# Kernel tuning notes

Measured on AMD Instinct MI355X. Metric: run time of the kernel, lower is better.

The kernel has to match this reference:

```python
import jax, jax.numpy as jnp
import numpy as np

B, C, H, W = 8, 128, 256, 256
WS = 8          # window_size (square)
HEADS = 4


def setup_inputs() -> dict:
    key = jax.random.key(0)
    k1, k2, k3, k4 = jax.random.split(key, 4)
    x = jax.random.normal(k1, (B, C, H, W), dtype=jnp.float32)
    # 1x1 convs are per-pixel matmuls; store weights as [out, in]
    w_qkv = jax.random.normal(k2, (3 * C, C), dtype=jnp.float32) * 0.05   # qkv conv, bias=False
    w_proj = jax.random.normal(k3, (C, C), dtype=jnp.float32) * 0.05      # proj conv weight
    b_proj = jax.random.normal(k4, (C,), dtype=jnp.float32) * 0.01        # proj conv bias
    return {"x": x, "w_qkv": w_qkv, "w_proj": w_proj, "b_proj": b_proj}


def reference(x, w_qkv, w_proj, b_proj):
    b, c, h, w = x.shape
    ws, heads = WS, HEADS
    d = c // heads
    scale = d ** -0.5
    hn, wn = h // ws, w // ws
    n = ws * ws  # tokens per window

    # unfold with kernel=stride=ws -> row-major window partition
    # [B,C,H,W] -> [B*hn*wn, C, n]
    xw = x.reshape(b, c, hn, ws, wn, ws)
    xw = xw.transpose(0, 2, 4, 1, 3, 5).reshape(b * hn * wn, c, n)

    # 1x1 conv QKV projection (no bias)
    qkv = jnp.einsum('oc,bcn->bon', w_qkv, xw)  # [Bw, 3C, n]
    q, k, v = jnp.split(qkv, 3, axis=1)
    q = q.reshape(-1, heads, d, n)
    k = k.reshape(-1, heads, d, n)
    v = v.reshape(-1, heads, d, n)

    # attn = (q^T k) * scale, softmax over keys
    attn = jax.nn.softmax(jnp.einsum('bhdn,bhdm->bhnm', q, k) * scale, axis=-1)
    out = jnp.einsum('bhnm,bhdm->bhdn', attn, v).reshape(-1, c, n)  # [Bw, C, n]

    # 1x1 proj conv with bias
    out = jnp.einsum('oc,bcn->bon', w_proj, out) + b_proj[None, :, None]

    # fold windows back: [Bw, C, n] -> [B, C, H, W]
    out = out.reshape(b, hn, wn, c, ws, ws)
    out = out.transpose(0, 3, 1, 4, 2, 5).reshape(b, c, h, w)
    return out
```

## Files before the change

### kernel.cpp

```cpp
#include <hip/hip_runtime.h>


#define HH    256
#define WWID  256
#define SCALE 0.17677669529663687f

typedef float  f32x4  __attribute__((ext_vector_type(4)));
typedef __bf16 bf16x8 __attribute__((ext_vector_type(8)));
typedef short  s16x4  __attribute__((ext_vector_type(4)));
typedef unsigned short ushort_t;

#define SCR_BASE 16384

__device__ __forceinline__ ushort_t f2bf(float x) {
  unsigned u = __float_as_uint(x);
  u += 0x7fffu + ((u >> 16) & 1u);
  return (ushort_t)(u >> 16);
}

__global__ void prep_weights(const float* __restrict__ wqkv,
                             const float* __restrict__ wproj,
                             ushort_t* __restrict__ wbf) {
  int i = blockIdx.x * 256 + threadIdx.x;
  float v = (i < 49152) ? wqkv[i] : wproj[i - 49152];
  wbf[i] = f2bf(v);
}

__global__ __launch_bounds__(256, 2)
void winattn_main(const float* __restrict__ x,
                  const ushort_t* __restrict__ wqkv,
                  const ushort_t* __restrict__ wproj,
                  const float* __restrict__ bproj,
                  float* __restrict__ out) {
  __shared__ __align__(16) char smem[32768];

  const int tid  = threadIdx.x;
  const int lane = tid & 63;
  const int wv   = tid >> 6;
  const int l15  = lane & 15;
  const int l4   = lane >> 4;

  const int bid = blockIdx.x;
  const int win = ((bid & 7) << 10) | (bid >> 3);
  const int b   = win >> 10;
  const int wy  = (win >> 5) & 31;
  const int wx  = win & 31;
  const int gy0 = wy * 8, gx0 = wx * 8;

  #pragma unroll
  for (int it = 0; it < 4; ++it) {
    int idx   = tid + it * 256;
    int cpair = idx >> 4;
    int r     = idx & 15;
    int ty    = r >> 1, tx4 = r & 1;
    const float* px = x + (((size_t)(b * 128 + 2 * cpair) * HH + gy0 + ty) * WWID + gx0 + tx4 * 4);
    float4 v0 = *(const float4*)px;
    float4 v1 = *(const float4*)(px + (size_t)HH * WWID);
    float a0[4] = {v0.x, v0.y, v0.z, v0.w};
    float a1[4] = {v1.x, v1.y, v1.z, v1.w};
    #pragma unroll
    for (int i = 0; i < 4; ++i) {
      int tok = ty * 8 + tx4 * 4 + i;
      unsigned wword = (unsigned)f2bf(a0[i]) | ((unsigned)f2bf(a1[i]) << 16);
      int byte = (tok * 256 + cpair * 4) ^ ((tok & 7) << 4);
      *(unsigned*)(smem + byte) = wword;
    }
  }
  __syncthreads();

  const int scr = SCR_BASE + wv * 4096;
  bf16x8 bk[4], aq[4], bv[2][2];

  #define XT_AFRAG(mt, kt) \
    (*(const bf16x8*)(smem + ((((mt) * 16 + l15) * 256 + ((kt) * 32 + l4 * 8) * 2) ^ \
                              ((((mt) * 16 + l15) & 7) << 4))))

  #pragma unroll
  for (int nt2 = 0; nt2 < 2; ++nt2) {
    int orow0 = 128 + wv * 32 + nt2 * 16;
    f32x4 acc[4] = {};
    #pragma unroll
    for (int kt = 0; kt < 4; ++kt) {
      bf16x8 bf = *(const bf16x8*)(wqkv + (size_t)(orow0 + l15) * 128 + kt * 32 + l4 * 8);
      #pragma unroll
      for (int mt = 0; mt < 4; ++mt)
        acc[mt] = __builtin_amdgcn_mfma_f32_16x16x32_bf16(XT_AFRAG(mt, kt), bf, acc[mt], 0, 0, 0);
    }
    int dloc = nt2 * 16 + l15;
    #pragma unroll
    for (int mt = 0; mt < 4; ++mt)
      #pragma unroll
      for (int r = 0; r < 4; ++r) {
        int tok  = mt * 16 + l4 * 4 + r;
        int byte = scr + ((tok * 64 + dloc * 2) ^ ((tok & 3) << 4));
        *(ushort_t*)(smem + byte) = f2bf(acc[mt][r]);
      }
  }
  #pragma unroll
  for (int mtS = 0; mtS < 4; ++mtS) {
    int m    = mtS * 16 + l15;
    int byte = scr + ((m * 64 + l4 * 16) ^ ((m & 3) << 4));
    bk[mtS] = *(const bf16x8*)(smem + byte);
  }
  #pragma unroll
  for (int nt2 = 0; nt2 < 2; ++nt2) {
    int orow0 = wv * 32 + nt2 * 16;
    f32x4 acc[4] = {};
    #pragma unroll
    for (int kt = 0; kt < 4; ++kt) {
      bf16x8 bf = *(const bf16x8*)(wqkv + (size_t)(orow0 + l15) * 128 + kt * 32 + l4 * 8);
      #pragma unroll
      for (int mt = 0; mt < 4; ++mt)
        acc[mt] = __builtin_amdgcn_mfma_f32_16x16x32_bf16(XT_AFRAG(mt, kt), bf, acc[mt], 0, 0, 0);
    }
    int dloc = nt2 * 16 + l15;
    #pragma unroll
    for (int mt = 0; mt < 4; ++mt)
      #pragma unroll
      for (int r = 0; r < 4; ++r) {
        int tok  = mt * 16 + l4 * 4 + r;
        int byte = scr + ((tok * 64 + dloc * 2) ^ ((tok & 3) << 4));
        *(ushort_t*)(smem + byte) = f2bf(acc[mt][r] * SCALE);
      }
  }
  #pragma unroll
  for (int t = 0; t < 4; ++t) {
    int tok  = t * 16 + l15;
    int byte = scr + ((tok * 64 + l4 * 16) ^ ((tok & 3) << 4));
    aq[t] = *(const bf16x8*)(smem + byte);
  }
  #pragma unroll
  for (int nt2 = 0; nt2 < 2; ++nt2) {
    int orow0 = 256 + wv * 32 + nt2 * 16;
    f32x4 acc[4] = {};
    #pragma unroll
    for (int kt = 0; kt < 4; ++kt) {
      bf16x8 bf = *(const bf16x8*)(wqkv + (size_t)(orow0 + l15) * 128 + kt * 32 + l4 * 8);
      #pragma unroll
      for (int mt = 0; mt < 4; ++mt)
        acc[mt] = __builtin_amdgcn_mfma_f32_16x16x32_bf16(XT_AFRAG(mt, kt), bf, acc[mt], 0, 0, 0);
    }
    int dloc = nt2 * 16 + l15;
    #pragma unroll
    for (int mt = 0; mt < 4; ++mt) {
      int tok0 = mt * 16 + l4 * 4;
      s16x4 wv4;
      #pragma unroll
      for (int r = 0; r < 4; ++r) wv4[r] = (short)f2bf(acc[mt][r]);
      int byte = scr + ((dloc * 128 + tok0 * 2) ^ ((dloc & 7) << 4));
      *(s16x4*)(smem + byte) = wv4;
    }
  }
  #pragma unroll
  for (int vt = 0; vt < 2; ++vt)
    #pragma unroll
    for (int kt = 0; kt < 2; ++kt) {
      int d    = vt * 16 + l15;
      int byte = scr + ((d * 128 + (kt * 32 + l4 * 8) * 2) ^ ((d & 7) << 4));
      bv[vt][kt] = *(const bf16x8*)(smem + byte);
    }

  f32x4 oacc[2][2][2] = {};
  #pragma unroll
  for (int hf = 0; hf < 2; ++hf) {
    #pragma unroll
    for (int qt = 0; qt < 2; ++qt) {
      f32x4 s[4];
      #pragma unroll
      for (int mtS = 0; mtS < 4; ++mtS) {
        f32x4 z = {0.f, 0.f, 0.f, 0.f};
        s[mtS] = __builtin_amdgcn_mfma_f32_16x16x32_bf16(aq[hf * 2 + qt], bk[mtS], z, 0, 0, 0);
      }
      #pragma unroll
      for (int r = 0; r < 4; ++r) {
        float v0 = s[0][r], v1 = s[1][r], v2 = s[2][r], v3 = s[3][r];
        float mx = fmaxf(fmaxf(v0, v1), fmaxf(v2, v3));
        mx = fmaxf(mx, __shfl_xor(mx, 1));
        mx = fmaxf(mx, __shfl_xor(mx, 2));
        mx = fmaxf(mx, __shfl_xor(mx, 4));
        mx = fmaxf(mx, __shfl_xor(mx, 8));
        float e0 = __expf(v0 - mx), e1 = __expf(v1 - mx);
        float e2 = __expf(v2 - mx), e3 = __expf(v3 - mx);
        float sm = e0 + e1 + e2 + e3;
        sm += __shfl_xor(sm, 1);
        sm += __shfl_xor(sm, 2);
        sm += __shfl_xor(sm, 4);
        sm += __shfl_xor(sm, 8);
        float inv = 1.0f / sm;
        int nl = qt * 16 + l4 * 4 + r;
        int sw = (nl & 7) << 4;
        *(ushort_t*)(smem + scr + ((nl * 128 + (0 * 16 + l15) * 2) ^ sw)) = f2bf(e0 * inv);
        *(ushort_t*)(smem + scr + ((nl * 128 + (1 * 16 + l15) * 2) ^ sw)) = f2bf(e1 * inv);
        *(ushort_t*)(smem + scr + ((nl * 128 + (2 * 16 + l15) * 2) ^ sw)) = f2bf(e2 * inv);
        *(ushort_t*)(smem + scr + ((nl * 128 + (3 * 16 + l15) * 2) ^ sw)) = f2bf(e3 * inv);
      }
    }
    #pragma unroll
    for (int kt = 0; kt < 2; ++kt)
      #pragma unroll
      for (int rt = 0; rt < 2; ++rt) {
        int nl   = rt * 16 + l15;
        int byte = scr + ((nl * 128 + (kt * 32 + l4 * 8) * 2) ^ ((nl & 7) << 4));
        bf16x8 ap = *(const bf16x8*)(smem + byte);
        #pragma unroll
        for (int vt = 0; vt < 2; ++vt)
          oacc[hf][rt][vt] =
              __builtin_amdgcn_mfma_f32_16x16x32_bf16(ap, bv[vt][kt], oacc[hf][rt][vt], 0, 0, 0);
      }
  }
  __syncthreads();

  #pragma unroll
  for (int hf = 0; hf < 2; ++hf)
    #pragma unroll
    for (int rt = 0; rt < 2; ++rt)
      #pragma unroll
      for (int vt = 0; vt < 2; ++vt)
        #pragma unroll
        for (int r = 0; r < 4; ++r) {
          int tok  = hf * 32 + rt * 16 + l4 * 4 + r;
          int c    = wv * 32 + vt * 16 + l15;
          int byte = (tok * 256 + c * 2) ^ ((tok & 7) << 4);
          *(ushort_t*)(smem + byte) = f2bf(oacc[hf][rt][vt][r]);
        }
  __syncthreads();

  f32x4 pacc[2][4];
  #pragma unroll
  for (int i = 0; i < 2; ++i) {
    #pragma unroll
    for (int mt = 0; mt < 4; ++mt) pacc[i][mt] = (f32x4){0.f, 0.f, 0.f, 0.f};
    int orow0 = (wv * 2 + i) * 16;
    #pragma unroll
    for (int kt = 0; kt < 4; ++kt) {
      bf16x8 bf = *(const bf16x8*)(wproj + (size_t)(orow0 + l15) * 128 + kt * 32 + l4 * 8);
      #pragma unroll
      for (int mt = 0; mt < 4; ++mt)
        pacc[i][mt] = __builtin_amdgcn_mfma_f32_16x16x32_bf16(XT_AFRAG(mt, kt), bf, pacc[i][mt], 0, 0, 0);
    }
  }

  #pragma unroll
  for (int half = 0; half < 2; ++half) {
    __syncthreads();
    #pragma unroll
    for (int i = 0; i < 2; ++i) {
      int o = (wv * 2 + i) * 16 + l15;
      #pragma unroll
      for (int m2 = 0; m2 < 2; ++m2)
        #pragma unroll
        for (int r = 0; r < 4; ++r) {
          int ytok = m2 * 16 + l4 * 4 + r;
          int byte = SCR_BASE + ((ytok * 512 + o * 4) ^ ((ytok & 7) << 4));
          *(float*)(smem + byte) = pacc[i][half * 2 + m2][r];
        }
    }
    __syncthreads();
    #pragma unroll
    for (int it = 0; it < 2; ++it) {
      int idx = tid + it * 256;
      int o   = idx & 127;
      int ty  = idx >> 7;
      float bias = bproj[o];
      float vals[8];
      #pragma unroll
      for (int tx = 0; tx < 8; ++tx) {
        int ytok = ty * 8 + tx;
        int byte = SCR_BASE + ((ytok * 512 + o * 4) ^ ((ytok & 7) << 4));
        vals[tx] = *(const float*)(smem + byte) + bias;
      }
      int row = half * 4 + ty;
      float4 f0 = {vals[0], vals[1], vals[2], vals[3]};
      float4 f1 = {vals[4], vals[5], vals[6], vals[7]};
      float* po = out + (((size_t)(b * 128 + o) * HH + gy0 + row) * WWID + gx0);
      *(float4*)po       = f0;
      *(float4*)(po + 4) = f1;
    }
  }
}

extern "C" void kernel_launch(void* const* d_in, const int* in_sizes, int n_in,
                              void* d_out, int out_size, void* d_ws, size_t ws_size,
                              hipStream_t stream) {
  const float* x     = (const float*)d_in[0];
  const float* wqkv  = (const float*)d_in[1];
  const float* wproj = (const float*)d_in[2];
  const float* bproj = (const float*)d_in[3];
  float* out = (float*)d_out;

  ushort_t* wbf = (ushort_t*)d_ws;
  prep_weights<<<256, 256, 0, stream>>>(wqkv, wproj, wbf);
  winattn_main<<<8192, 256, 0, stream>>>(x, wbf, wbf + 49152, bproj, out);
}
```

Baseline: 297.6 us.

## Fuse Q/K projection, transpose MFMA operands, and write output directly from accumulators

Computes Q and K projections in one pass that shares the x fragments, and swaps the MFMA operand order so accumulator lanes hold contiguous token runs. That enables vectorized bf16x4 LDS stores and a softmax that reduces in registers with only two cross-lane shuffles. The attention scale is folded into the Q weights during weight prep, and native __bf16 conversions replace manual rounding. The projection epilogue now writes float4 values straight to global memory, removing the LDS staging round trip and its barriers. The cost is higher register pressure from holding accQ and accK together, plus less coalesced output stores.

```diff
diff --git a/kernel.cpp b/kernel.cpp
--- a/kernel.cpp
+++ b/kernel.cpp
@@ -7,29 +7,24 @@
 
 typedef float  f32x4  __attribute__((ext_vector_type(4)));
 typedef __bf16 bf16x8 __attribute__((ext_vector_type(8)));
-typedef short  s16x4  __attribute__((ext_vector_type(4)));
-typedef unsigned short ushort_t;
+typedef __bf16 bf16x4 __attribute__((ext_vector_type(4)));
+typedef __bf16 bf16x2 __attribute__((ext_vector_type(2)));
 
 #define SCR_BASE 16384
-
-__device__ __forceinline__ ushort_t f2bf(float x) {
-  unsigned u = __float_as_uint(x);
-  u += 0x7fffu + ((u >> 16) & 1u);
-  return (ushort_t)(u >> 16);
-}
 
 __global__ void prep_weights(const float* __restrict__ wqkv,
                              const float* __restrict__ wproj,
-                             ushort_t* __restrict__ wbf) {
+                             __bf16* __restrict__ wbf) {
   int i = blockIdx.x * 256 + threadIdx.x;
   float v = (i < 49152) ? wqkv[i] : wproj[i - 49152];
-  wbf[i] = f2bf(v);
+  if (i < 16384) v *= SCALE;
+  wbf[i] = (__bf16)v;
 }
 
 __global__ __launch_bounds__(256, 2)
 void winattn_main(const float* __restrict__ x,
-                  const ushort_t* __restrict__ wqkv,
-                  const ushort_t* __restrict__ wproj,
+                  const __bf16* __restrict__ wqkv,
+                  const __bf16* __restrict__ wproj,
                   const float* __restrict__ bproj,
                   float* __restrict__ out) {
   __shared__ __align__(16) char smem[32768];
@@ -61,9 +56,9 @@
     #pragma unroll
     for (int i = 0; i < 4; ++i) {
       int tok = ty * 8 + tx4 * 4 + i;
-      unsigned wword = (unsigned)f2bf(a0[i]) | ((unsigned)f2bf(a1[i]) << 16);
+      bf16x2 w2 = {(__bf16)a0[i], (__bf16)a1[i]};
       int byte = (tok * 256 + cpair * 4) ^ ((tok & 7) << 4);
-      *(unsigned*)(smem + byte) = wword;
+      *(bf16x2*)(smem + byte) = w2;
     }
   }
   __syncthreads();
@@ -75,124 +70,133 @@
     (*(const bf16x8*)(smem + ((((mt) * 16 + l15) * 256 + ((kt) * 32 + l4 * 8) * 2) ^ \
                               ((((mt) * 16 + l15) & 7) << 4))))
 
-  #pragma unroll
-  for (int nt2 = 0; nt2 < 2; ++nt2) {
-    int orow0 = 128 + wv * 32 + nt2 * 16;
-    f32x4 acc[4] = {};
+  {
+    f32x4 accQ[2][4] = {}, accK[2][4] = {};
     #pragma unroll
     for (int kt = 0; kt < 4; ++kt) {
-      bf16x8 bf = *(const bf16x8*)(wqkv + (size_t)(orow0 + l15) * 128 + kt * 32 + l4 * 8);
-      #pragma unroll
-      for (int mt = 0; mt < 4; ++mt)
-        acc[mt] = __builtin_amdgcn_mfma_f32_16x16x32_bf16(XT_AFRAG(mt, kt), bf, acc[mt], 0, 0, 0);
-    }
-    int dloc = nt2 * 16 + l15;
-    #pragma unroll
-    for (int mt = 0; mt < 4; ++mt)
-      #pragma unroll
-      for (int r = 0; r < 4; ++r) {
-        int tok  = mt * 16 + l4 * 4 + r;
-        int byte = scr + ((tok * 64 + dloc * 2) ^ ((tok & 3) << 4));
-        *(ushort_t*)(smem + byte) = f2bf(acc[mt][r]);
-      }
-  }
-  #pragma unroll
-  for (int mtS = 0; mtS < 4; ++mtS) {
-    int m    = mtS * 16 + l15;
-    int byte = scr + ((m * 64 + l4 * 16) ^ ((m & 3) << 4));
-    bk[mtS] = *(const bf16x8*)(smem + byte);
-  }
-  #pragma unroll
-  for (int nt2 = 0; nt2 < 2; ++nt2) {
-    int orow0 = wv * 32 + nt2 * 16;
-    f32x4 acc[4] = {};
+      bf16x8 xf[4];
+      #pragma unroll
+      for (int mt = 0; mt < 4; ++mt) xf[mt] = XT_AFRAG(mt, kt);
+      #pragma unroll
+      for (int nt2 = 0; nt2 < 2; ++nt2) {
+        bf16x8 wq = *(const bf16x8*)(wqkv + (size_t)(wv * 32 + nt2 * 16 + l15) * 128 + kt * 32 + l4 * 8);
+        bf16x8 wk = *(const bf16x8*)(wqkv + (size_t)(128 + wv * 32 + nt2 * 16 + l15) * 128 + kt * 32 + l4 * 8);
+        #pragma unroll
+        for (int mt = 0; mt < 4; ++mt) {
+          accQ[nt2][mt] = __builtin_amdgcn_mfma_f32_16x16x32_bf16(wq, xf[mt], accQ[nt2][mt], 0, 0, 0);
+          accK[nt2][mt] = __builtin_amdgcn_mfma_f32_16x16x32_bf16(wk, xf[mt], accK[nt2][mt], 0, 0, 0);
+        }
+      }
+    }
+    #pragma unroll
+    for (int nt2 = 0; nt2 < 2; ++nt2)
+      #pragma unroll
+      for (int mt = 0; mt < 4; ++mt) {
+        int tok = mt * 16 + l15;
+        bf16x4 kp = {(__bf16)accK[nt2][mt][0], (__bf16)accK[nt2][mt][1],
+                     (__bf16)accK[nt2][mt][2], (__bf16)accK[nt2][mt][3]};
+        int byte = scr + ((tok * 64 + (nt2 * 16 + l4 * 4) * 2) ^ ((tok & 3) << 4));
+        *(bf16x4*)(smem + byte) = kp;
+      }
+    #pragma unroll
+    for (int mtS = 0; mtS < 4; ++mtS) {
+      int m    = mtS * 16 + l15;
+      int byte = scr + ((m * 64 + l4 * 16) ^ ((m & 3) << 4));
+      bk[mtS] = *(const bf16x8*)(smem + byte);
+    }
+    #pragma unroll
+    for (int nt2 = 0; nt2 < 2; ++nt2)
+      #pragma unroll
+      for (int mt = 0; mt < 4; ++mt) {
+        int tok = mt * 16 + l15;
+        bf16x4 qp = {(__bf16)accQ[nt2][mt][0], (__bf16)accQ[nt2][mt][1],
+                     (__bf16)accQ[nt2][mt][2], (__bf16)accQ[nt2][mt][3]};
+        int byte = scr + ((tok * 64 + (nt2 * 16 + l4 * 4) * 2) ^ ((tok & 3) << 4));
+        *(bf16x4*)(smem + byte) = qp;
+      }
+    #pragma unroll
+    for (int t = 0; t < 4; ++t) {
+      int tok  = t * 16 + l15;
+      int byte = scr + ((tok * 64 + l4 * 16) ^ ((tok & 3) << 4));
+      aq[t] = *(const bf16x8*)(smem + byte);
+    }
+  }
+
+  {
+    f32x4 accV[2][4] = {};
     #pragma unroll
     for (int kt = 0; kt < 4; ++kt) {
-      bf16x8 bf = *(const bf16x8*)(wqkv + (size_t)(orow0 + l15) * 128 + kt * 32 + l4 * 8);
-      #pragma unroll
-      for (int mt = 0; mt < 4; ++mt)
-        acc[mt] = __builtin_amdgcn_mfma_f32_16x16x32_bf16(XT_AFRAG(mt, kt), bf, acc[mt], 0, 0, 0);
-    }
-    int dloc = nt2 * 16 + l15;
-    #pragma unroll
-    for (int mt = 0; mt < 4; ++mt)
-      #pragma unroll
-      for (int r = 0; r < 4; ++r) {
-        int tok  = mt * 16 + l4 * 4 + r;
-        int byte = scr + ((tok * 64 + dloc * 2) ^ ((tok & 3) << 4));
-        *(ushort_t*)(smem + byte) = f2bf(acc[mt][r] * SCALE);
-      }
-  }
-  #pragma unroll
-  for (int t = 0; t < 4; ++t) {
-    int tok  = t * 16 + l15;
-    int byte = scr + ((tok * 64 + l4 * 16) ^ ((tok & 3) << 4));
-    aq[t] = *(const bf16x8*)(smem + byte);
-  }
-  #pragma unroll
-  for (int nt2 = 0; nt2 < 2; ++nt2) {
-    int orow0 = 256 + wv * 32 + nt2 * 16;
-    f32x4 acc[4] = {};
-    #pragma unroll
-    for (int kt = 0; kt < 4; ++kt) {
-      bf16x8 bf = *(const bf16x8*)(wqkv + (size_t)(orow0 + l15) * 128 + kt * 32 + l4 * 8);
-      #pragma unroll
-      for (int mt = 0; mt < 4; ++mt)
-        acc[mt] = __builtin_amdgcn_mfma_f32_16x16x32_bf16(XT_AFRAG(mt, kt), bf, acc[mt], 0, 0, 0);
-    }
-    int dloc = nt2 * 16 + l15;
-    #pragma unroll
-    for (int mt = 0; mt < 4; ++mt) {
-      int tok0 = mt * 16 + l4 * 4;
-      s16x4 wv4;
-      #pragma unroll
-      for (int r = 0; r < 4; ++r) wv4[r] = (short)f2bf(acc[mt][r]);
-      int byte = scr + ((dloc * 128 + tok0 * 2) ^ ((dloc & 7) << 4));
-      *(s16x4*)(smem + byte) = wv4;
-    }
-  }
-  #pragma unroll
-  for (int vt = 0; vt < 2; ++vt)
-    #pragma unroll
-    for (int kt = 0; kt < 2; ++kt) {
-      int d    = vt * 16 + l15;
-      int byte = scr + ((d * 128 + (kt * 32 + l4 * 8) * 2) ^ ((d & 7) << 4));
-      bv[vt][kt] = *(const bf16x8*)(smem + byte);
-    }
+      bf16x8 xf[4];
+      #pragma unroll
+      for (int mt = 0; mt < 4; ++mt) xf[mt] = XT_AFRAG(mt, kt);
+      #pragma unroll
+      for (int nt2 = 0; nt2 < 2; ++nt2) {
+        bf16x8 wf = *(const bf16x8*)(wqkv + (size_t)(256 + wv * 32 + nt2 * 16 + l15) * 128 + kt * 32 + l4 * 8);
+        #pragma unroll
+        for (int mt = 0; mt < 4; ++mt)
+          accV[nt2][mt] = __builtin_amdgcn_mfma_f32_16x16x32_bf16(xf[mt], wf, accV[nt2][mt], 0, 0, 0);
+      }
+    }
+    #pragma unroll
+    for (int nt2 = 0; nt2 < 2; ++nt2) {
+      int dloc = nt2 * 16 + l15;
+      #pragma unroll
+      for (int mt = 0; mt < 4; ++mt) {
+        int tok0 = mt * 16 + l4 * 4;
+        bf16x4 vp = {(__bf16)accV[nt2][mt][0], (__bf16)accV[nt2][mt][1],
+                     (__bf16)accV[nt2][mt][2], (__bf16)accV[nt2][mt][3]};
+        int byte = scr + ((dloc * 128 + tok0 * 2) ^ ((dloc & 7) << 4));
+        *(bf16x4*)(smem + byte) = vp;
+      }
+    }
+    #pragma unroll
+    for (int vt = 0; vt < 2; ++vt)
+      #pragma unroll
+      for (int kt = 0; kt < 2; ++kt) {
+        int d    = vt * 16 + l15;
+        int byte = scr + ((d * 128 + (kt * 32 + l4 * 8) * 2) ^ ((d & 7) << 4));
+        bv[vt][kt] = *(const bf16x8*)(smem + byte);
+      }
+  }
 
   f32x4 oacc[2][2][2] = {};
   #pragma unroll
   for (int hf = 0; hf < 2; ++hf) {
     #pragma unroll
     for (int qt = 0; qt < 2; ++qt) {
-      f32x4 s[4];
+      f32x4 st[4];
       #pragma unroll
       for (int mtS = 0; mtS < 4; ++mtS) {
         f32x4 z = {0.f, 0.f, 0.f, 0.f};
-        s[mtS] = __builtin_amdgcn_mfma_f32_16x16x32_bf16(aq[hf * 2 + qt], bk[mtS], z, 0, 0, 0);
-      }
-      #pragma unroll
-      for (int r = 0; r < 4; ++r) {
-        float v0 = s[0][r], v1 = s[1][r], v2 = s[2][r], v3 = s[3][r];
-        float mx = fmaxf(fmaxf(v0, v1), fmaxf(v2, v3));
-        mx = fmaxf(mx, __shfl_xor(mx, 1));
-        mx = fmaxf(mx, __shfl_xor(mx, 2));
-        mx = fmaxf(mx, __shfl_xor(mx, 4));
-        mx = fmaxf(mx, __shfl_xor(mx, 8));
-        float e0 = __expf(v0 - mx), e1 = __expf(v1 - mx);
-        float e2 = __expf(v2 - mx), e3 = __expf(v3 - mx);
-        float sm = e0 + e1 + e2 + e3;
-        sm += __shfl_xor(sm, 1);
-        sm += __shfl_xor(sm, 2);
-        sm += __shfl_xor(sm, 4);
-        sm += __shfl_xor(sm, 8);
-        float inv = 1.0f / sm;
-        int nl = qt * 16 + l4 * 4 + r;
-        int sw = (nl & 7) << 4;
-        *(ushort_t*)(smem + scr + ((nl * 128 + (0 * 16 + l15) * 2) ^ sw)) = f2bf(e0 * inv);
-        *(ushort_t*)(smem + scr + ((nl * 128 + (1 * 16 + l15) * 2) ^ sw)) = f2bf(e1 * inv);
-        *(ushort_t*)(smem + scr + ((nl * 128 + (2 * 16 + l15) * 2) ^ sw)) = f2bf(e2 * inv);
-        *(ushort_t*)(smem + scr + ((nl * 128 + (3 * 16 + l15) * 2) ^ sw)) = f2bf(e3 * inv);
+        st[mtS] = __builtin_amdgcn_mfma_f32_16x16x32_bf16(bk[mtS], aq[hf * 2 + qt], z, 0, 0, 0);
+      }
+      float mx = st[0][0];
+      #pragma unroll
+      for (int mtS = 0; mtS < 4; ++mtS)
+        #pragma unroll
+        for (int r = 0; r < 4; ++r) mx = fmaxf(mx, st[mtS][r]);
+      mx = fmaxf(mx, __shfl_xor(mx, 16));
+      mx = fmaxf(mx, __shfl_xor(mx, 32));
+      float p[4][4];
+      float sm = 0.f;
+      #pragma unroll
+      for (int mtS = 0; mtS < 4; ++mtS)
+        #pragma unroll
+        for (int r = 0; r < 4; ++r) {
+          p[mtS][r] = __expf(st[mtS][r] - mx);
+          sm += p[mtS][r];
+        }
+      sm += __shfl_xor(sm, 16);
+      sm += __shfl_xor(sm, 32);
+      float inv = 1.0f / sm;
+      int qrow = qt * 16 + l15;
+      int sw   = (qrow & 7) << 4;
+      #pragma unroll
+      for (int mtS = 0; mtS < 4; ++mtS) {
+        bf16x4 pp = {(__bf16)(p[mtS][0] * inv), (__bf16)(p[mtS][1] * inv),
+                     (__bf16)(p[mtS][2] * inv), (__bf16)(p[mtS][3] * inv)};
+        int byte = scr + ((qrow * 128 + (mtS * 16 + l4 * 4) * 2) ^ sw);
+        *(bf16x4*)(smem + byte) = pp;
       }
     }
     #pragma unroll
@@ -221,60 +225,37 @@
           int tok  = hf * 32 + rt * 16 + l4 * 4 + r;
           int c    = wv * 32 + vt * 16 + l15;
           int byte = (tok * 256 + c * 2) ^ ((tok & 7) << 4);
-          *(ushort_t*)(smem + byte) = f2bf(oacc[hf][rt][vt][r]);
+          *(__bf16*)(smem + byte) = (__bf16)oacc[hf][rt][vt][r];
         }
   __syncthreads();
 
-  f32x4 pacc[2][4];
+  f32x4 pacc[2][4] = {};
+  #pragma unroll
+  for (int kt = 0; kt < 4; ++kt) {
+    bf16x8 of[4];
+    #pragma unroll
+    for (int mt = 0; mt < 4; ++mt) of[mt] = XT_AFRAG(mt, kt);
+    #pragma unroll
+    for (int i = 0; i < 2; ++i) {
+      bf16x8 wp = *(const bf16x8*)(wproj + (size_t)((wv * 2 + i) * 16 + l15) * 128 + kt * 32 + l4 * 8);
+      #pragma unroll
+      for (int mt = 0; mt < 4; ++mt)
+        pacc[i][mt] = __builtin_amdgcn_mfma_f32_16x16x32_bf16(of[mt], wp, pacc[i][mt], 0, 0, 0);
+    }
+  }
+
   #pragma unroll
   for (int i = 0; i < 2; ++i) {
-    #pragma unroll
-    for (int mt = 0; mt < 4; ++mt) pacc[i][mt] = (f32x4){0.f, 0.f, 0.f, 0.f};
-    int orow0 = (wv * 2 + i) * 16;
-    #pragma unroll
-    for (int kt = 0; kt < 4; ++kt) {
-      bf16x8 bf = *(const bf16x8*)(wproj + (size_t)(orow0 + l15) * 128 + kt * 32 + l4 * 8);
-      #pragma unroll
-      for (int mt = 0; mt < 4; ++mt)
-        pacc[i][mt] = __builtin_amdgcn_mfma_f32_16x16x32_bf16(XT_AFRAG(mt, kt), bf, pacc[i][mt], 0, 0, 0);
-    }
-  }
-
-  #pragma unroll
-  for (int half = 0; half < 2; ++half) {
-    __syncthreads();
-    #pragma unroll
-    for (int i = 0; i < 2; ++i) {
-      int o = (wv * 2 + i) * 16 + l15;
-      #pragma unroll
-      for (int m2 = 0; m2 < 2; ++m2)
-        #pragma unroll
-        for (int r = 0; r < 4; ++r) {
-          int ytok = m2 * 16 + l4 * 4 + r;
-          int byte = SCR_BASE + ((ytok * 512 + o * 4) ^ ((ytok & 7) << 4));
-          *(float*)(smem + byte) = pacc[i][half * 2 + m2][r];
-        }
-    }
-    __syncthreads();
-    #pragma unroll
-    for (int it = 0; it < 2; ++it) {
-      int idx = tid + it * 256;
-      int o   = idx & 127;
-      int ty  = idx >> 7;
-      float bias = bproj[o];
-      float vals[8];
-      #pragma unroll
-      for (int tx = 0; tx < 8; ++tx) {
-        int ytok = ty * 8 + tx;
-        int byte = SCR_BASE + ((ytok * 512 + o * 4) ^ ((ytok & 7) << 4));
-        vals[tx] = *(const float*)(smem + byte) + bias;
-      }
-      int row = half * 4 + ty;
-      float4 f0 = {vals[0], vals[1], vals[2], vals[3]};
-      float4 f1 = {vals[4], vals[5], vals[6], vals[7]};
-      float* po = out + (((size_t)(b * 128 + o) * HH + gy0 + row) * WWID + gx0);
-      *(float4*)po       = f0;
-      *(float4*)(po + 4) = f1;
+    int o = (wv * 2 + i) * 16 + l15;
+    float bias = bproj[o];
+    float* obase = out + (size_t)(b * 128 + o) * ((size_t)HH * WWID) + gy0 * WWID + gx0;
+    #pragma unroll
+    for (int mt = 0; mt < 4; ++mt) {
+      int tok0 = mt * 16 + l4 * 4;
+      int ty = tok0 >> 3, tx0 = tok0 & 7;
+      float4 f = {pacc[i][mt][0] + bias, pacc[i][mt][1] + bias,
+                  pacc[i][mt][2] + bias, pacc[i][mt][3] + bias};
+      *(float4*)(obase + ty * WWID + tx0) = f;
     }
   }
 }
@@ -288,7 +269,7 @@
   const float* bproj = (const float*)d_in[3];
   float* out = (float*)d_out;
 
-  ushort_t* wbf = (ushort_t*)d_ws;
+  __bf16* wbf = (__bf16*)d_ws;
   prep_weights<<<256, 256, 0, stream>>>(wqkv, wproj, wbf);
   winattn_main<<<8192, 256, 0, stream>>>(x, wbf, wbf + 49152, bproj, out);
 }
```

New measurement: 253.4 us. 1.17x faster.
